# Performance work log

Hardware: AMD Instinct MI355X
Metric: run time of the kernel (lower is better)

The kernel has to match this reference:

```python
import jax, jax.numpy as jnp
import numpy as np

CH_IN = 256
CH_OUT = 32


def setup_inputs() -> dict:
    key = jax.random.key(0)
    ks = jax.random.split(key, 7)
    b, c, H, W = 4, CH_IN, 64, 64
    x = jax.random.normal(ks[0], (b, c, H, W), dtype=jnp.float32)
    # 1x1 conv weights (out, in) and biases, small init like torch default
    sc_in = 1.0 / np.sqrt(CH_IN)
    Wf = jax.random.uniform(ks[1], (CH_OUT, CH_IN), jnp.float32, -sc_in, sc_in)
    bf = jax.random.uniform(ks[2], (CH_OUT,), jnp.float32, -sc_in, sc_in)
    Wg = jax.random.uniform(ks[3], (CH_OUT, CH_IN), jnp.float32, -sc_in, sc_in)
    bg = jax.random.uniform(ks[4], (CH_OUT,), jnp.float32, -sc_in, sc_in)
    Wh = jax.random.uniform(ks[5], (CH_IN, CH_IN), jnp.float32, -sc_in, sc_in)
    bh = jax.random.uniform(ks[6], (CH_IN,), jnp.float32, -sc_in, sc_in)
    return {"x": x, "Wf": Wf, "bf": bf, "Wg": Wg, "bg": bg, "Wh": Wh, "bh": bh}


def reference(x, Wf, bf, Wg, bg, Wh, bh):
    b, c, H, W = x.shape
    xf = x.reshape(b, c, H * W)                      # [b, c, N]
    # 1x1 convs == per-pixel linear projections
    f = jnp.einsum('oc,bcn->bon', Wf, xf) + bf[None, :, None]   # [b, ch_out, N]
    g = jnp.einsum('oc,bcn->bon', Wg, xf) + bg[None, :, None]   # [b, ch_out, N]
    h = jnp.einsum('oc,bcn->bon', Wh, xf) + bh[None, :, None]   # [b, ch_in, N]
    # s[b, i, j] = sum_o f[b,o,i] * g[b,o,j]
    s = jnp.einsum('boi,boj->bij', f, g)             # [b, N, N]
    # torch softmax over dim=1 (the i axis)
    beta = jax.nn.softmax(s, axis=1)                 # [b, N, N]
    # o = h @ beta : [b, c, N] x [b, N, N] -> [b, c, N]
    o = jnp.einsum('bcn,bnm->bcm', h, beta)
    return o.reshape(b, c, H, W)
```

## Files before the change

### kernel.cpp

```cpp
#include <hip/hip_runtime.h>
#include <hip/hip_bf16.h>
#include <math.h>

#define BATCH 4
#define CIN   256
#define DQK   32
#define NPIX  4096
#define MTOT  320

typedef __attribute__((ext_vector_type(4))) float f32x4;
typedef __attribute__((ext_vector_type(8))) short bf16x8;
typedef __attribute__((ext_vector_type(4))) unsigned int u32x4;

__device__ __forceinline__ unsigned short f2bf(float f) {
  unsigned u = __builtin_bit_cast(unsigned, f);
  u += 0x7FFFu + ((u >> 16) & 1u);
  return (unsigned short)(u >> 16);
}
__device__ __forceinline__ unsigned pk2(float a, float b) {
  return (unsigned)f2bf(a) | ((unsigned)f2bf(b) << 16);
}
__device__ __forceinline__ void barrier_lds() {
  asm volatile("s_waitcnt lgkmcnt(0)" ::: "memory");
  __builtin_amdgcn_s_barrier();
  asm volatile("" ::: "memory");
}

__global__ void wcvt(const float* __restrict__ Wh, const float* __restrict__ Wf,
                     const float* __restrict__ Wg,
                     const float* __restrict__ bh, const float* __restrict__ bf,
                     const float* __restrict__ bg,
                     unsigned short* __restrict__ Wb, float* __restrict__ bcat) {
  const int r = blockIdx.x;
  const int c = threadIdx.x;
  const float* src = (r < 256) ? &Wh[r * CIN] : (r < 288) ? &Wf[(r - 256) * CIN] : &Wg[(r - 288) * CIN];
  Wb[r * CIN + c] = f2bf(src[c]);
  if (c == 0)
    bcat[r] = (r < 256) ? bh[r] : (r < 288) ? bf[r - 256] : bg[r - 288];
}

#define XPAD 4
__launch_bounds__(512, 1)
__global__ void proj_all(const float* __restrict__ x, const unsigned short* __restrict__ Wb,
                         const float* __restrict__ bcat,
                         unsigned short* __restrict__ F, unsigned short* __restrict__ G,
                         unsigned short* __restrict__ H) {
  __shared__ unsigned short Xs[64 * (CIN + XPAD)];

  const int bid = blockIdx.x;
  const int b = bid >> 6;
  const int n0 = (bid & 63) << 6;
  const int t = threadIdx.x;
  const int lane = t & 63;
  const int w = t >> 6;

  const float* __restrict__ xb = x + (size_t)b * CIN * NPIX + n0;
#pragma unroll
  for (int p = 0; p < 16; ++p) {
    const int k = p * 16 + w * 2;
    const float a0 = xb[(size_t)k * NPIX + lane];
    const float a1 = xb[(size_t)(k + 1) * NPIX + lane];
    const unsigned pk = (unsigned)f2bf(a0) | ((unsigned)f2bf(a1) << 16);
    *(unsigned*)((char*)Xs + lane * (CIN + XPAD) * 2 + k * 2) = pk;
  }
  __syncthreads();

  const int l16 = lane & 15, lhi = lane >> 4;
  const int wm = w >> 1;
  const int wn = w & 1;

  const f32x4 fzero = {0.f, 0.f, 0.f, 0.f};
  f32x4 acc[5][2];
#pragma unroll
  for (int i = 0; i < 5; ++i)
#pragma unroll
    for (int j = 0; j < 2; ++j) acc[i][j] = fzero;

#pragma unroll
  for (int ks = 0; ks < 8; ++ks) {
    bf16x8 bx[2];
#pragma unroll
    for (int j = 0; j < 2; ++j)
      bx[j] = *(const bf16x8*)&Xs[(wn * 32 + j * 16 + l16) * (CIN + XPAD) + ks * 32 + lhi * 8];
#pragma unroll
    for (int i = 0; i < 5; ++i) {
      const bf16x8 aw = *(const bf16x8*)(Wb + (size_t)(wm * 80 + i * 16 + l16) * CIN + ks * 32 + lhi * 8);
#pragma unroll
      for (int j = 0; j < 2; ++j)
        acc[i][j] = __builtin_amdgcn_mfma_f32_16x16x32_bf16(aw, bx[j], acc[i][j], 0, 0, 0);
    }
  }

#pragma unroll
  for (int i = 0; i < 5; ++i) {
    const int MT = wm * 5 + i;
    const int m0 = MT * 16;
    const f32x4 bias = *(const f32x4*)&bcat[m0 + lhi * 4];
#pragma unroll
    for (int j = 0; j < 2; ++j) {
      const int n = n0 + wn * 32 + j * 16 + l16;
      f32x4 v = acc[i][j];
      v.x += bias.x; v.y += bias.y; v.z += bias.z; v.w += bias.w;
      if (MT < 16) {
        const int c0 = m0 + lhi * 4;
        unsigned short* dst = H + ((size_t)b * CIN + c0) * NPIX + n;
        dst[0 * NPIX] = f2bf(v.x);
        dst[1 * NPIX] = f2bf(v.y);
        dst[2 * NPIX] = f2bf(v.z);
        dst[3 * NPIX] = f2bf(v.w);
      } else {
        unsigned short* dst = (MT < 18) ? F : G;
        const int d0 = ((MT - 16) & 1) * 16 + lhi * 4;
        uint2 pk;
        pk.x = (unsigned)f2bf(v.x) | ((unsigned)f2bf(v.y) << 16);
        pk.y = (unsigned)f2bf(v.z) | ((unsigned)f2bf(v.w) << 16);
        *(uint2*)(dst + ((size_t)b * NPIX + n) * DQK + d0) = pk;
      }
    }
  }
}

#define BNK  64
#define KEYS 2048
#define NTILE (KEYS / BNK)

__launch_bounds__(256, 2)
__global__ void attn_split(const unsigned short* __restrict__ F,
                           const unsigned short* __restrict__ G,
                           const unsigned short* __restrict__ H,
                           unsigned short* __restrict__ Ap, float* __restrict__ Lp) {
  __shared__ unsigned short Kl[2][64][36];
  __shared__ unsigned short Pl[2][64][72];

  const int bid = blockIdx.x;
  const int b = (bid & 7) >> 1;
  const int split = bid & 1;
  const int qt = bid >> 3;
  const int t = threadIdx.x;
  const int lane = t & 63, cs = t >> 6;
  const int l16 = lane & 15, lhi = lane >> 4;

  const unsigned short* Fb = F + (size_t)b * NPIX * DQK;
  const unsigned short* Gb = G + (size_t)b * NPIX * DQK;
  const unsigned short* Hb = H + (size_t)b * CIN * NPIX;
  const int nb0 = split * KEYS;
  const int q0 = qt * 64;

  const f32x4 fzero = {0.f, 0.f, 0.f, 0.f};

  bf16x8 qf[4];
#pragma unroll
  for (int mt = 0; mt < 4; ++mt)
    qf[mt] = *(const bf16x8*)(Gb + (size_t)(q0 + mt * 16 + l16) * DQK + lhi * 8);

  f32x4 acc[4][4];
#pragma unroll
  for (int ct = 0; ct < 4; ++ct)
#pragma unroll
    for (int mt = 0; mt < 4; ++mt) acc[ct][mt] = fzero;
  float Lacc[4] = {0.f, 0.f, 0.f, 0.f};

  const int krow = t >> 2, kslot = t & 3;
  const unsigned short* Kg = Fb + ((size_t)(nb0 + krow)) * DQK + kslot * 8;
  const unsigned short* vp[4];
#pragma unroll
  for (int ct = 0; ct < 4; ++ct)
    vp[ct] = Hb + (size_t)(cs * 64 + ct * 16 + l16) * NPIX + nb0 + lhi * 8;

  u32x4 kr;
  kr = *(const u32x4*)Kg;
  *(u32x4*)&Kl[0][krow][kslot * 8] = kr;
  kr = *(const u32x4*)(Kg + 1 * BNK * DQK);
  barrier_lds();

  for (int tt = 0; tt < NTILE; ++tt) {
    const int buf = tt & 1;
    u32x4 vr[8];
#pragma unroll
    for (int ct = 0; ct < 4; ++ct)
#pragma unroll
      for (int kk = 0; kk < 2; ++kk)
        vr[ct * 2 + kk] = *(const u32x4*)(vp[ct] + (size_t)tt * BNK + kk * 32);
    if (tt + 1 < NTILE) *(u32x4*)&Kl[buf ^ 1][krow][kslot * 8] = kr;
    if (tt + 2 < NTILE) kr = *(const u32x4*)(Kg + (size_t)(tt + 2) * BNK * DQK);

    const bf16x8 kf = *(const bf16x8*)&Kl[buf][cs * 16 + l16][lhi * 8];
    f32x4 s_[4];
#pragma unroll
    for (int mt = 0; mt < 4; ++mt)
      s_[mt] = __builtin_amdgcn_mfma_f32_16x16x32_bf16(kf, qf[mt], fzero, 0, 0, 0);

#pragma unroll
    for (int mt = 0; mt < 4; ++mt) {
      const float p0 = __expf(s_[mt][0]), p1 = __expf(s_[mt][1]);
      const float p2 = __expf(s_[mt][2]), p3 = __expf(s_[mt][3]);
      Lacc[mt] += (p0 + p1) + (p2 + p3);
      uint2 pk; pk.x = pk2(p0, p1); pk.y = pk2(p2, p3);
      *(uint2*)&Pl[buf][mt * 16 + l16][cs * 16 + lhi * 4] = pk;
    }
    barrier_lds();

    __builtin_amdgcn_s_setprio(1);
#pragma unroll
    for (int kk = 0; kk < 2; ++kk) {
      bf16x8 pf[4];
#pragma unroll
      for (int mt = 0; mt < 4; ++mt)
        pf[mt] = *(const bf16x8*)&Pl[buf][mt * 16 + l16][kk * 32 + lhi * 8];
#pragma unroll
      for (int ct = 0; ct < 4; ++ct) {
        const bf16x8 vf = __builtin_bit_cast(bf16x8, vr[ct * 2 + kk]);
#pragma unroll
        for (int mt = 0; mt < 4; ++mt)
          acc[ct][mt] = __builtin_amdgcn_mfma_f32_16x16x32_bf16(vf, pf[mt], acc[ct][mt], 0, 0, 0);
      }
    }
    __builtin_amdgcn_s_setprio(0);
  }

#pragma unroll
  for (int mt = 0; mt < 4; ++mt) {
    float L = Lacc[mt];
    L += __shfl_xor(L, 16, 64);
    L += __shfl_xor(L, 32, 64);
    if (lhi == 0)
      Lp[((size_t)split * 4 + cs) * (4 * NPIX) + (size_t)b * NPIX + q0 + mt * 16 + l16] = L;
  }
#pragma unroll
  for (int ct = 0; ct < 4; ++ct)
#pragma unroll
    for (int mt = 0; mt < 4; ++mt) {
      const int c = cs * 64 + ct * 16 + lhi * 4;
      const int q = q0 + mt * 16 + l16;
      unsigned short* dst = Ap + (((size_t)split * 4 + b) * CIN + c) * NPIX + q;
#pragma unroll
      for (int v = 0; v < 4; ++v) dst[(size_t)v * NPIX] = f2bf(acc[ct][mt][v]);
    }
}

__global__ void combineL(const float* __restrict__ Lp, float* __restrict__ Linv) {
  const int idx = blockIdx.x * 256 + threadIdx.x;
  float s = 0.f;
#pragma unroll
  for (int i = 0; i < 8; ++i) s += Lp[(size_t)i * (4 * NPIX) + idx];
  Linv[idx] = 1.f / s;
}

__global__ void combine(const unsigned short* __restrict__ Ap, const float* __restrict__ Linv,
                        float* __restrict__ out) {
  const size_t base = ((size_t)blockIdx.x * 256 + threadIdx.x) * 8;
  const int b = (int)(base / ((size_t)CIN * NPIX));
  const int q = (int)(base % NPIX);
  const u32x4 a0 = *(const u32x4*)(Ap + base);
  const u32x4 a1 = *(const u32x4*)(Ap + (size_t)4 * CIN * NPIX + base);
  const float* lv = &Linv[(size_t)b * NPIX + q];
  float r[8];
#pragma unroll
  for (int i = 0; i < 4; ++i) {
    const float x0 = __builtin_bit_cast(float, (a0[i] & 0xFFFFu) << 16) +
                     __builtin_bit_cast(float, (a1[i] & 0xFFFFu) << 16);
    const float x1 = __builtin_bit_cast(float, (a0[i] & 0xFFFF0000u)) +
                     __builtin_bit_cast(float, (a1[i] & 0xFFFF0000u));
    r[2 * i] = x0 * lv[2 * i];
    r[2 * i + 1] = x1 * lv[2 * i + 1];
  }
  *(f32x4*)&out[base] = *(f32x4*)&r[0];
  *(f32x4*)&out[base + 4] = *(f32x4*)&r[4];
}

#define BN 32
__launch_bounds__(512, 2)
__global__ void attn_kernel(const unsigned short* __restrict__ F,
                            const unsigned short* __restrict__ G,
                            const unsigned short* __restrict__ H,
                            float* __restrict__ out) {
  __shared__ unsigned short Klds[32 * 40];
  __shared__ unsigned short Vlds[256 * 40];
  __shared__ unsigned short Plds[8][32 * 40];

  const int bid = blockIdx.x;
  const int b = bid >> 6;
  const int t = threadIdx.x;
  const int lane = t & 63;
  const int w = t >> 6;
  const int l16 = lane & 15;
  const int lhi = lane >> 4;
  const int m0 = ((bid & 63) << 6) + ((w >> 2) << 5);
  const int c0 = (w & 3) << 6;

  const f32x4 fzero = {0.f, 0.f, 0.f, 0.f};

  bf16x8 qf[2];
#pragma unroll
  for (int mt = 0; mt < 2; ++mt)
    qf[mt] = *(const bf16x8*)(G + ((size_t)b * NPIX + m0 + mt * 16 + l16) * DQK + lhi * 8);

  f32x4 acc[4][2];
#pragma unroll
  for (int ct = 0; ct < 4; ++ct)
#pragma unroll
    for (int mt = 0; mt < 2; ++mt) acc[ct][mt] = fzero;
  float Mr[2] = {-INFINITY, -INFINITY};
  float Lr[2] = {0.f, 0.f};

  const unsigned short* Fb = F + (size_t)b * NPIX * DQK;
  const unsigned short* Hb = H + (size_t)b * CIN * NPIX;
  unsigned short* Pw = &Plds[w][0];

  for (int n0 = 0; n0 < NPIX; n0 += BN) {
    __syncthreads();
    if (t < 128) {
      const int nr = t >> 2, sl = t & 3;
      *(u32x4*)&Klds[nr * 40 + sl * 8] = *(const u32x4*)(Fb + (size_t)(n0 + nr) * DQK + sl * 8);
    }
#pragma unroll
    for (int i = 0; i < 2; ++i) {
      const int q = t + i * 512;
      const int cr = q >> 2, sl = q & 3;
      *(u32x4*)&Vlds[cr * 40 + sl * 8] = *(const u32x4*)(Hb + (size_t)cr * NPIX + n0 + sl * 8);
    }
    __syncthreads();

    bf16x8 kf[2];
#pragma unroll
    for (int nts = 0; nts < 2; ++nts)
      kf[nts] = *(const bf16x8*)&Klds[(nts * 16 + l16) * 40 + lhi * 8];
    f32x4 s[2][2];
#pragma unroll
    for (int mt = 0; mt < 2; ++mt)
#pragma unroll
      for (int nts = 0; nts < 2; ++nts)
        s[mt][nts] = __builtin_amdgcn_mfma_f32_16x16x32_bf16(kf[nts], qf[mt], fzero, 0, 0, 0);

#pragma unroll
    for (int mt = 0; mt < 2; ++mt) {
      float tmax = s[mt][0][0];
#pragma unroll
      for (int v = 1; v < 4; ++v) tmax = fmaxf(tmax, s[mt][0][v]);
#pragma unroll
      for (int v = 0; v < 4; ++v) tmax = fmaxf(tmax, s[mt][1][v]);
      tmax = fmaxf(tmax, __shfl_xor(tmax, 16, 64));
      tmax = fmaxf(tmax, __shfl_xor(tmax, 32, 64));
      const float newM = fmaxf(Mr[mt], tmax);
      const float rescale = __expf(Mr[mt] - newM);
      Mr[mt] = newM;
      float p[2][4];
      float psum = 0.f;
#pragma unroll
      for (int nts = 0; nts < 2; ++nts)
#pragma unroll
        for (int v = 0; v < 4; ++v) {
          p[nts][v] = __expf(s[mt][nts][v] - newM);
          psum += p[nts][v];
        }
      psum += __shfl_xor(psum, 16, 64);
      psum += __shfl_xor(psum, 32, 64);
      Lr[mt] = Lr[mt] * rescale + psum;
#pragma unroll
      for (int ct = 0; ct < 4; ++ct) acc[ct][mt] *= rescale;
#pragma unroll
      for (int nts = 0; nts < 2; ++nts) {
        uint2 pkv;
        pkv.x = (unsigned)f2bf(p[nts][0]) | ((unsigned)f2bf(p[nts][1]) << 16);
        pkv.y = (unsigned)f2bf(p[nts][2]) | ((unsigned)f2bf(p[nts][3]) << 16);
        *(uint2*)&Pw[(mt * 16 + l16) * 40 + nts * 16 + lhi * 4] = pkv;
      }
    }
    asm volatile("" ::: "memory");

    bf16x8 pf[2];
#pragma unroll
    for (int mt = 0; mt < 2; ++mt)
      pf[mt] = *(const bf16x8*)&Pw[(mt * 16 + l16) * 40 + lhi * 8];
#pragma unroll
    for (int ct = 0; ct < 4; ++ct) {
      const bf16x8 vf = *(const bf16x8*)&Vlds[(c0 + ct * 16 + l16) * 40 + lhi * 8];
#pragma unroll
      for (int mt = 0; mt < 2; ++mt)
        acc[ct][mt] = __builtin_amdgcn_mfma_f32_16x16x32_bf16(vf, pf[mt], acc[ct][mt], 0, 0, 0);
    }
  }

#pragma unroll
  for (int mt = 0; mt < 2; ++mt) {
    const float invL = 1.f / Lr[mt];
    const int m = m0 + mt * 16 + l16;
#pragma unroll
    for (int ct = 0; ct < 4; ++ct)
#pragma unroll
      for (int v = 0; v < 4; ++v) {
        const int c = c0 + ct * 16 + lhi * 4 + v;
        out[((size_t)b * CIN + c) * NPIX + m] = acc[ct][mt][v] * invL;
      }
  }
}

extern "C" void kernel_launch(void* const* d_in, const int* in_sizes, int n_in,
                              void* d_out, int out_size, void* d_ws, size_t ws_size,
                              hipStream_t stream) {
  (void)in_sizes; (void)n_in; (void)out_size;
  const float* x  = (const float*)d_in[0];
  const float* Wf = (const float*)d_in[1];
  const float* bf = (const float*)d_in[2];
  const float* Wg = (const float*)d_in[3];
  const float* bg = (const float*)d_in[4];
  const float* Wh = (const float*)d_in[5];
  const float* bh = (const float*)d_in[6];
  float* out = (float*)d_out;

  unsigned short* Fw = (unsigned short*)d_ws;
  unsigned short* Gw = Fw + (size_t)BATCH * NPIX * DQK;
  unsigned short* Hw = Gw + (size_t)BATCH * NPIX * DQK;
  unsigned short* Wb = Hw + (size_t)BATCH * CIN * NPIX;
  float* bcat = (float*)(Wb + (size_t)MTOT * CIN);
  unsigned short* Apart = (unsigned short*)(bcat + MTOT);
  float* Lpart = (float*)(Apart + (size_t)2 * BATCH * CIN * NPIX);
  float* Linv  = Lpart + (size_t)8 * BATCH * NPIX;
  const size_t NEED = (size_t)((char*)(Linv + (size_t)BATCH * NPIX) - (char*)d_ws);

  hipLaunchKernelGGL(wcvt, dim3(MTOT), dim3(256), 0, stream, Wh, Wf, Wg, bh, bf, bg, Wb, bcat);
  hipLaunchKernelGGL(proj_all, dim3(BATCH * 64), dim3(512), 0, stream, x, Wb, bcat, Fw, Gw, Hw);

  if (ws_size >= NEED) {
    hipLaunchKernelGGL(attn_split, dim3(BATCH * 64 * 2), dim3(256), 0, stream, Fw, Gw, Hw, Apart, Lpart);
    hipLaunchKernelGGL(combineL, dim3(BATCH * NPIX / 256), dim3(256), 0, stream, Lpart, Linv);
    hipLaunchKernelGGL(combine, dim3((size_t)BATCH * CIN * NPIX / 8 / 256), dim3(256), 0, stream, Apart, Linv, out);
  } else {
    hipLaunchKernelGGL(attn_kernel, dim3(BATCH * 64), dim3(512), 0, stream, Fw, Gw, Hw, out);
  }
}
```

Baseline: 99.10 us.

## Stage V tiles in shared LDS across two query-group waves per block

```diff
diff --git a/kernel.cpp b/kernel.cpp
--- a/kernel.cpp
+++ b/kernel.cpp
@@ -124,102 +124,104 @@
 #define KEYS 2048
 #define NTILE (KEYS / BNK)
 
-__launch_bounds__(256, 2)
+__launch_bounds__(512, 4)
 __global__ void attn_split(const unsigned short* __restrict__ F,
                            const unsigned short* __restrict__ G,
                            const unsigned short* __restrict__ H,
                            unsigned short* __restrict__ Ap, float* __restrict__ Lp) {
-  __shared__ unsigned short Kl[2][64][36];
-  __shared__ unsigned short Pl[2][64][72];
+  __shared__ unsigned short Kl[64][36];
+  __shared__ unsigned short Vl[256][72];
+  __shared__ unsigned short Pl[2][32][72];
 
   const int bid = blockIdx.x;
-  const int b = (bid & 7) >> 1;
+  const int b = (bid >> 1) & 3;
   const int split = bid & 1;
   const int qt = bid >> 3;
   const int t = threadIdx.x;
-  const int lane = t & 63, cs = t >> 6;
+  const int lane = t & 63, w = t >> 6;
   const int l16 = lane & 15, lhi = lane >> 4;
+  const int mg = w >> 2, cs = w & 3;
 
   const unsigned short* Fb = F + (size_t)b * NPIX * DQK;
   const unsigned short* Gb = G + (size_t)b * NPIX * DQK;
   const unsigned short* Hb = H + (size_t)b * CIN * NPIX;
   const int nb0 = split * KEYS;
-  const int q0 = qt * 64;
+  const int q0 = qt * 64 + mg * 32;
 
   const f32x4 fzero = {0.f, 0.f, 0.f, 0.f};
 
-  bf16x8 qf[4];
-#pragma unroll
-  for (int mt = 0; mt < 4; ++mt)
+  bf16x8 qf[2];
+#pragma unroll
+  for (int mt = 0; mt < 2; ++mt)
     qf[mt] = *(const bf16x8*)(Gb + (size_t)(q0 + mt * 16 + l16) * DQK + lhi * 8);
 
-  f32x4 acc[4][4];
+  f32x4 acc[4][2];
 #pragma unroll
   for (int ct = 0; ct < 4; ++ct)
 #pragma unroll
-    for (int mt = 0; mt < 4; ++mt) acc[ct][mt] = fzero;
-  float Lacc[4] = {0.f, 0.f, 0.f, 0.f};
-
+    for (int mt = 0; mt < 2; ++mt) acc[ct][mt] = fzero;
+  float Lacc[2] = {0.f, 0.f};
+
+  const int vrow = t >> 3, vslot = t & 7;
   const int krow = t >> 2, kslot = t & 3;
-  const unsigned short* Kg = Fb + ((size_t)(nb0 + krow)) * DQK + kslot * 8;
-  const unsigned short* vp[4];
-#pragma unroll
-  for (int ct = 0; ct < 4; ++ct)
-    vp[ct] = Hb + (size_t)(cs * 64 + ct * 16 + l16) * NPIX + nb0 + lhi * 8;
-
-  u32x4 kr;
-  kr = *(const u32x4*)Kg;
-  *(u32x4*)&Kl[0][krow][kslot * 8] = kr;
-  kr = *(const u32x4*)(Kg + 1 * BNK * DQK);
-  barrier_lds();
+  const unsigned short* Vg = Hb + (size_t)vrow * NPIX + nb0 + vslot * 8;
+  const unsigned short* Kg = Fb + (size_t)(nb0 + krow) * DQK + kslot * 8;
+
+  u32x4 vr[4];
+  u32x4 kr = {0, 0, 0, 0};
+
+#pragma unroll
+  for (int i = 0; i < 4; ++i)
+    vr[i] = *(const u32x4*)(Vg + (size_t)i * 64 * NPIX);
+  if (t < 256) kr = *(const u32x4*)Kg;
 
   for (int tt = 0; tt < NTILE; ++tt) {
-    const int buf = tt & 1;
-    u32x4 vr[8];
-#pragma unroll
-    for (int ct = 0; ct < 4; ++ct)
-#pragma unroll
-      for (int kk = 0; kk < 2; ++kk)
-        vr[ct * 2 + kk] = *(const u32x4*)(vp[ct] + (size_t)tt * BNK + kk * 32);
-    if (tt + 1 < NTILE) *(u32x4*)&Kl[buf ^ 1][krow][kslot * 8] = kr;
-    if (tt + 2 < NTILE) kr = *(const u32x4*)(Kg + (size_t)(tt + 2) * BNK * DQK);
-
-    const bf16x8 kf = *(const bf16x8*)&Kl[buf][cs * 16 + l16][lhi * 8];
-    f32x4 s_[4];
-#pragma unroll
-    for (int mt = 0; mt < 4; ++mt)
+#pragma unroll
+    for (int i = 0; i < 4; ++i)
+      *(u32x4*)&Vl[i * 64 + vrow][vslot * 8] = vr[i];
+    if (t < 256) *(u32x4*)&Kl[krow][kslot * 8] = kr;
+    barrier_lds();
+    if (tt + 1 < NTILE) {
+#pragma unroll
+      for (int i = 0; i < 4; ++i)
+        vr[i] = *(const u32x4*)(Vg + (size_t)i * 64 * NPIX + (size_t)(tt + 1) * BNK);
+      if (t < 256) kr = *(const u32x4*)(Kg + (size_t)(tt + 1) * BNK * DQK);
+    }
+    const bf16x8 kf = *(const bf16x8*)&Kl[cs * 16 + l16][lhi * 8];
+    f32x4 s_[2];
+#pragma unroll
+    for (int mt = 0; mt < 2; ++mt)
       s_[mt] = __builtin_amdgcn_mfma_f32_16x16x32_bf16(kf, qf[mt], fzero, 0, 0, 0);
-
-#pragma unroll
-    for (int mt = 0; mt < 4; ++mt) {
+#pragma unroll
+    for (int mt = 0; mt < 2; ++mt) {
       const float p0 = __expf(s_[mt][0]), p1 = __expf(s_[mt][1]);
       const float p2 = __expf(s_[mt][2]), p3 = __expf(s_[mt][3]);
       Lacc[mt] += (p0 + p1) + (p2 + p3);
       uint2 pk; pk.x = pk2(p0, p1); pk.y = pk2(p2, p3);
-      *(uint2*)&Pl[buf][mt * 16 + l16][cs * 16 + lhi * 4] = pk;
+      *(uint2*)&Pl[mg][mt * 16 + l16][cs * 16 + lhi * 4] = pk;
     }
     barrier_lds();
-
     __builtin_amdgcn_s_setprio(1);
 #pragma unroll
     for (int kk = 0; kk < 2; ++kk) {
-      bf16x8 pf[4];
-#pragma unroll
-      for (int mt = 0; mt < 4; ++mt)
-        pf[mt] = *(const bf16x8*)&Pl[buf][mt * 16 + l16][kk * 32 + lhi * 8];
+      bf16x8 pf[2];
+#pragma unroll
+      for (int mt = 0; mt < 2; ++mt)
+        pf[mt] = *(const bf16x8*)&Pl[mg][mt * 16 + l16][kk * 32 + lhi * 8];
 #pragma unroll
       for (int ct = 0; ct < 4; ++ct) {
-        const bf16x8 vf = __builtin_bit_cast(bf16x8, vr[ct * 2 + kk]);
-#pragma unroll
-        for (int mt = 0; mt < 4; ++mt)
+        const bf16x8 vf = *(const bf16x8*)&Vl[cs * 64 + ct * 16 + l16][kk * 32 + lhi * 8];
+#pragma unroll
+        for (int mt = 0; mt < 2; ++mt)
           acc[ct][mt] = __builtin_amdgcn_mfma_f32_16x16x32_bf16(vf, pf[mt], acc[ct][mt], 0, 0, 0);
       }
     }
     __builtin_amdgcn_s_setprio(0);
-  }
-
-#pragma unroll
-  for (int mt = 0; mt < 4; ++mt) {
+    barrier_lds();
+  }
+
+#pragma unroll
+  for (int mt = 0; mt < 2; ++mt) {
     float L = Lacc[mt];
     L += __shfl_xor(L, 16, 64);
     L += __shfl_xor(L, 32, 64);
@@ -229,7 +231,7 @@
 #pragma unroll
   for (int ct = 0; ct < 4; ++ct)
 #pragma unroll
-    for (int mt = 0; mt < 4; ++mt) {
+    for (int mt = 0; mt < 2; ++mt) {
       const int c = cs * 64 + ct * 16 + lhi * 4;
       const int q = q0 + mt * 16 + l16;
       unsigned short* dst = Ap + (((size_t)split * 4 + b) * CIN + c) * NPIX + q;
@@ -422,7 +424,7 @@
   hipLaunchKernelGGL(proj_all, dim3(BATCH * 64), dim3(512), 0, stream, x, Wb, bcat, Fw, Gw, Hw);
 
   if (ws_size >= NEED) {
-    hipLaunchKernelGGL(attn_split, dim3(BATCH * 64 * 2), dim3(256), 0, stream, Fw, Gw, Hw, Apart, Lpart);
+    hipLaunchKernelGGL(attn_split, dim3(BATCH * 64 * 2), dim3(512), 0, stream, Fw, Gw, Hw, Apart, Lpart);
     hipLaunchKernelGGL(combineL, dim3(BATCH * NPIX / 256), dim3(256), 0, stream, Lpart, Linv);
     hipLaunchKernelGGL(combine, dim3((size_t)BATCH * CIN * NPIX / 8 / 256), dim3(256), 0, stream, Apart, Linv, out);
   } else {
```

Measured after the change: 95.29 us. 1.04x faster.

## Load K fragments directly to registers and double-buffer V/K register prefetch

Applied to the files above, without the earlier changes.

```diff
diff --git a/kernel.cpp b/kernel.cpp
--- a/kernel.cpp
+++ b/kernel.cpp
@@ -129,11 +129,10 @@
                            const unsigned short* __restrict__ G,
                            const unsigned short* __restrict__ H,
                            unsigned short* __restrict__ Ap, float* __restrict__ Lp) {
-  __shared__ unsigned short Kl[2][64][36];
-  __shared__ unsigned short Pl[2][64][72];
+  __shared__ unsigned short Pl[64][72];
 
   const int bid = blockIdx.x;
-  const int b = (bid & 7) >> 1;
+  const int b = (bid >> 1) & 3;
   const int split = bid & 1;
   const int qt = bid >> 3;
   const int t = threadIdx.x;
@@ -160,63 +159,66 @@
     for (int mt = 0; mt < 4; ++mt) acc[ct][mt] = fzero;
   float Lacc[4] = {0.f, 0.f, 0.f, 0.f};
 
-  const int krow = t >> 2, kslot = t & 3;
-  const unsigned short* Kg = Fb + ((size_t)(nb0 + krow)) * DQK + kslot * 8;
-  const unsigned short* vp[4];
+  const unsigned short* Kp = Fb + (size_t)(nb0 + cs * 16 + l16) * DQK + lhi * 8;
+  const unsigned short* Vp[4];
 #pragma unroll
   for (int ct = 0; ct < 4; ++ct)
-    vp[ct] = Hb + (size_t)(cs * 64 + ct * 16 + l16) * NPIX + nb0 + lhi * 8;
-
-  u32x4 kr;
-  kr = *(const u32x4*)Kg;
-  *(u32x4*)&Kl[0][krow][kslot * 8] = kr;
-  kr = *(const u32x4*)(Kg + 1 * BNK * DQK);
-  barrier_lds();
-
-  for (int tt = 0; tt < NTILE; ++tt) {
-    const int buf = tt & 1;
-    u32x4 vr[8];
-#pragma unroll
-    for (int ct = 0; ct < 4; ++ct)
-#pragma unroll
-      for (int kk = 0; kk < 2; ++kk)
-        vr[ct * 2 + kk] = *(const u32x4*)(vp[ct] + (size_t)tt * BNK + kk * 32);
-    if (tt + 1 < NTILE) *(u32x4*)&Kl[buf ^ 1][krow][kslot * 8] = kr;
-    if (tt + 2 < NTILE) kr = *(const u32x4*)(Kg + (size_t)(tt + 2) * BNK * DQK);
-
-    const bf16x8 kf = *(const bf16x8*)&Kl[buf][cs * 16 + l16][lhi * 8];
-    f32x4 s_[4];
-#pragma unroll
-    for (int mt = 0; mt < 4; ++mt)
-      s_[mt] = __builtin_amdgcn_mfma_f32_16x16x32_bf16(kf, qf[mt], fzero, 0, 0, 0);
-
-#pragma unroll
-    for (int mt = 0; mt < 4; ++mt) {
-      const float p0 = __expf(s_[mt][0]), p1 = __expf(s_[mt][1]);
-      const float p2 = __expf(s_[mt][2]), p3 = __expf(s_[mt][3]);
-      Lacc[mt] += (p0 + p1) + (p2 + p3);
-      uint2 pk; pk.x = pk2(p0, p1); pk.y = pk2(p2, p3);
-      *(uint2*)&Pl[buf][mt * 16 + l16][cs * 16 + lhi * 4] = pk;
-    }
-    barrier_lds();
-
-    __builtin_amdgcn_s_setprio(1);
-#pragma unroll
-    for (int kk = 0; kk < 2; ++kk) {
-      bf16x8 pf[4];
-#pragma unroll
-      for (int mt = 0; mt < 4; ++mt)
-        pf[mt] = *(const bf16x8*)&Pl[buf][mt * 16 + l16][kk * 32 + lhi * 8];
-#pragma unroll
-      for (int ct = 0; ct < 4; ++ct) {
-        const bf16x8 vf = __builtin_bit_cast(bf16x8, vr[ct * 2 + kk]);
-#pragma unroll
-        for (int mt = 0; mt < 4; ++mt)
-          acc[ct][mt] = __builtin_amdgcn_mfma_f32_16x16x32_bf16(vf, pf[mt], acc[ct][mt], 0, 0, 0);
-      }
-    }
-    __builtin_amdgcn_s_setprio(0);
-  }
+    Vp[ct] = Hb + (size_t)(cs * 64 + ct * 16 + l16) * NPIX + nb0 + lhi * 8;
+
+  u32x4 vA[8], vB[8], kA, kB;
+
+#define LOADT(VR, KR, TT) do {                                                       \
+    _Pragma("unroll")                                                                \
+    for (int ct_ = 0; ct_ < 4; ++ct_)                                                \
+      _Pragma("unroll")                                                              \
+      for (int kk_ = 0; kk_ < 2; ++kk_)                                              \
+        VR[ct_ * 2 + kk_] = *(const u32x4*)(Vp[ct_] + (size_t)(TT) * BNK + kk_ * 32);\
+    KR = *(const u32x4*)(Kp + (size_t)(TT) * BNK * DQK);                             \
+  } while (0)
+
+#define COMPUTE(VR, KR) do {                                                         \
+    const bf16x8 kf_ = __builtin_bit_cast(bf16x8, KR);                               \
+    f32x4 s_[4];                                                                     \
+    _Pragma("unroll")                                                                \
+    for (int mt_ = 0; mt_ < 4; ++mt_)                                                \
+      s_[mt_] = __builtin_amdgcn_mfma_f32_16x16x32_bf16(kf_, qf[mt_], fzero, 0, 0, 0);\
+    _Pragma("unroll")                                                                \
+    for (int mt_ = 0; mt_ < 4; ++mt_) {                                              \
+      const float p0 = __expf(s_[mt_][0]), p1 = __expf(s_[mt_][1]);                  \
+      const float p2 = __expf(s_[mt_][2]), p3 = __expf(s_[mt_][3]);                  \
+      Lacc[mt_] += (p0 + p1) + (p2 + p3);                                            \
+      uint2 pk_; pk_.x = pk2(p0, p1); pk_.y = pk2(p2, p3);                           \
+      *(uint2*)&Pl[mt_ * 16 + l16][cs * 16 + lhi * 4] = pk_;                         \
+    }                                                                                \
+    barrier_lds();                                                \
+    __builtin_amdgcn_s_setprio(1);                                                   \
+    _Pragma("unroll")                                                                \
+    for (int kk_ = 0; kk_ < 2; ++kk_) {                                              \
+      bf16x8 pf_[4];                                                                 \
+      _Pragma("unroll")                                                              \
+      for (int mt_ = 0; mt_ < 4; ++mt_)                                              \
+        pf_[mt_] = *(const bf16x8*)&Pl[mt_ * 16 + l16][kk_ * 32 + lhi * 8];          \
+      _Pragma("unroll")                                                              \
+      for (int ct_ = 0; ct_ < 4; ++ct_) {                                            \
+        const bf16x8 vf_ = __builtin_bit_cast(bf16x8, VR[ct_ * 2 + kk_]);            \
+        _Pragma("unroll")                                                            \
+        for (int mt_ = 0; mt_ < 4; ++mt_)                                            \
+          acc[ct_][mt_] = __builtin_amdgcn_mfma_f32_16x16x32_bf16(vf_, pf_[mt_], acc[ct_][mt_], 0, 0, 0); \
+      }                                                                              \
+    }                                                                                \
+    __builtin_amdgcn_s_setprio(0);                                                   \
+    barrier_lds();                          \
+  } while (0)
+
+  LOADT(vA, kA, 0);
+  for (int tt = 0; tt < NTILE; tt += 2) {
+    if (tt + 1 < NTILE) LOADT(vB, kB, tt + 1);
+    COMPUTE(vA, kA);
+    if (tt + 2 < NTILE) LOADT(vA, kA, tt + 2);
+    COMPUTE(vB, kB);
+  }
+#undef LOADT
+#undef COMPUTE
 
 #pragma unroll
   for (int mt = 0; mt < 4; ++mt) {
```

Result: slower. 107.7 us (+8.7%).

## Stage V tiles in LDS shared by two query groups and software-pipeline QK

Applied to the files above, without the earlier changes.

```diff
diff --git a/kernel.cpp b/kernel.cpp
--- a/kernel.cpp
+++ b/kernel.cpp
@@ -124,27 +124,30 @@
 #define KEYS 2048
 #define NTILE (KEYS / BNK)
 
-__launch_bounds__(256, 2)
+__launch_bounds__(512, 2)
 __global__ void attn_split(const unsigned short* __restrict__ F,
                            const unsigned short* __restrict__ G,
                            const unsigned short* __restrict__ H,
                            unsigned short* __restrict__ Ap, float* __restrict__ Lp) {
-  __shared__ unsigned short Kl[2][64][36];
-  __shared__ unsigned short Pl[2][64][72];
+  __shared__ unsigned short Kl[2][64][40];
+  __shared__ unsigned short Vl[2][256][72];
+  __shared__ unsigned short Pl[2][2][64][72];
 
   const int bid = blockIdx.x;
-  const int b = (bid & 7) >> 1;
-  const int split = bid & 1;
+  const int slab = bid & 7;
+  const int b = slab >> 1;
+  const int split = slab & 1;
   const int qt = bid >> 3;
   const int t = threadIdx.x;
-  const int lane = t & 63, cs = t >> 6;
+  const int lane = t & 63, w = t >> 6;
   const int l16 = lane & 15, lhi = lane >> 4;
+  const int mg = w >> 2, cs = w & 3;
 
   const unsigned short* Fb = F + (size_t)b * NPIX * DQK;
   const unsigned short* Gb = G + (size_t)b * NPIX * DQK;
   const unsigned short* Hb = H + (size_t)b * CIN * NPIX;
   const int nb0 = split * KEYS;
-  const int q0 = qt * 64;
+  const int q0 = qt * 128 + mg * 64;
 
   const f32x4 fzero = {0.f, 0.f, 0.f, 0.f};
 
@@ -160,63 +163,78 @@
     for (int mt = 0; mt < 4; ++mt) acc[ct][mt] = fzero;
   float Lacc[4] = {0.f, 0.f, 0.f, 0.f};
 
+  const int vrow = t >> 3, vslot = t & 7;
   const int krow = t >> 2, kslot = t & 3;
-  const unsigned short* Kg = Fb + ((size_t)(nb0 + krow)) * DQK + kslot * 8;
-  const unsigned short* vp[4];
-#pragma unroll
-  for (int ct = 0; ct < 4; ++ct)
-    vp[ct] = Hb + (size_t)(cs * 64 + ct * 16 + l16) * NPIX + nb0 + lhi * 8;
-
-  u32x4 kr;
-  kr = *(const u32x4*)Kg;
-  *(u32x4*)&Kl[0][krow][kslot * 8] = kr;
-  kr = *(const u32x4*)(Kg + 1 * BNK * DQK);
+  const unsigned short* Vg = Hb + (size_t)vrow * NPIX + nb0 + vslot * 8;
+  const unsigned short* Kg = Fb + (size_t)(nb0 + krow) * DQK + kslot * 8;
+
+  u32x4 vr[4];
+  u32x4 kr = {0, 0, 0, 0};
+
+#define LOADT(TT) do {                                                          \
+    _Pragma("unroll")                                                           \
+    for (int i_ = 0; i_ < 4; ++i_)                                              \
+      vr[i_] = *(const u32x4*)(Vg + (size_t)i_ * 64 * NPIX + (size_t)(TT) * BNK);\
+    if (t < 256) kr = *(const u32x4*)(Kg + (size_t)(TT) * BNK * DQK);           \
+  } while (0)
+
+#define STORET(BUF) do {                                                        \
+    _Pragma("unroll")                                                           \
+    for (int i_ = 0; i_ < 4; ++i_)                                              \
+      *(u32x4*)&Vl[BUF][i_ * 64 + vrow][vslot * 8] = vr[i_];                    \
+    if (t < 256) *(u32x4*)&Kl[BUF][krow][kslot * 8] = kr;                       \
+  } while (0)
+
+#define QKSM(BUF, PAR) do {                                                     \
+    const bf16x8 kf_ = *(const bf16x8*)&Kl[BUF][cs * 16 + l16][lhi * 8];        \
+    f32x4 s_[4];                                                                \
+    _Pragma("unroll")                                                           \
+    for (int mt_ = 0; mt_ < 4; ++mt_)                                           \
+      s_[mt_] = __builtin_amdgcn_mfma_f32_16x16x32_bf16(kf_, qf[mt_], fzero, 0, 0, 0); \
+    _Pragma("unroll")                                                           \
+    for (int mt_ = 0; mt_ < 4; ++mt_) {                                         \
+      const float p0 = __expf(s_[mt_][0]), p1 = __expf(s_[mt_][1]);             \
+      const float p2 = __expf(s_[mt_][2]), p3 = __expf(s_[mt_][3]);             \
+      Lacc[mt_] += (p0 + p1) + (p2 + p3);                                       \
+      uint2 pk_; pk_.x = pk2(p0, p1); pk_.y = pk2(p2, p3);                      \
+      *(uint2*)&Pl[PAR][mg][mt_ * 16 + l16][cs * 16 + lhi * 4] = pk_;           \
+    }                                                                           \
+  } while (0)
+
+  LOADT(0); STORET(0);
+  LOADT(1); STORET(1);
+  LOADT(2);
   barrier_lds();
+  QKSM(0, 0);
 
   for (int tt = 0; tt < NTILE; ++tt) {
     const int buf = tt & 1;
-    u32x4 vr[8];
-#pragma unroll
-    for (int ct = 0; ct < 4; ++ct)
+    barrier_lds();
+    bf16x8 pf[4][2];
+#pragma unroll
+    for (int mt = 0; mt < 4; ++mt)
 #pragma unroll
       for (int kk = 0; kk < 2; ++kk)
-        vr[ct * 2 + kk] = *(const u32x4*)(vp[ct] + (size_t)tt * BNK + kk * 32);
-    if (tt + 1 < NTILE) *(u32x4*)&Kl[buf ^ 1][krow][kslot * 8] = kr;
-    if (tt + 2 < NTILE) kr = *(const u32x4*)(Kg + (size_t)(tt + 2) * BNK * DQK);
-
-    const bf16x8 kf = *(const bf16x8*)&Kl[buf][cs * 16 + l16][lhi * 8];
-    f32x4 s_[4];
-#pragma unroll
-    for (int mt = 0; mt < 4; ++mt)
-      s_[mt] = __builtin_amdgcn_mfma_f32_16x16x32_bf16(kf, qf[mt], fzero, 0, 0, 0);
-
-#pragma unroll
-    for (int mt = 0; mt < 4; ++mt) {
-      const float p0 = __expf(s_[mt][0]), p1 = __expf(s_[mt][1]);
-      const float p2 = __expf(s_[mt][2]), p3 = __expf(s_[mt][3]);
-      Lacc[mt] += (p0 + p1) + (p2 + p3);
-      uint2 pk; pk.x = pk2(p0, p1); pk.y = pk2(p2, p3);
-      *(uint2*)&Pl[buf][mt * 16 + l16][cs * 16 + lhi * 4] = pk;
-    }
+        pf[mt][kk] = *(const bf16x8*)&Pl[buf][mg][mt * 16 + l16][kk * 32 + lhi * 8];
+    if (tt + 1 < NTILE) QKSM(buf ^ 1, buf ^ 1);
+    __builtin_amdgcn_s_setprio(1);
+#pragma unroll
+    for (int kk = 0; kk < 2; ++kk)
+#pragma unroll
+      for (int ct = 0; ct < 4; ++ct) {
+        const bf16x8 vf = *(const bf16x8*)&Vl[buf][cs * 64 + ct * 16 + l16][kk * 32 + lhi * 8];
+#pragma unroll
+        for (int mt = 0; mt < 4; ++mt)
+          acc[ct][mt] = __builtin_amdgcn_mfma_f32_16x16x32_bf16(vf, pf[mt][kk], acc[ct][mt], 0, 0, 0);
+      }
+    __builtin_amdgcn_s_setprio(0);
     barrier_lds();
-
-    __builtin_amdgcn_s_setprio(1);
-#pragma unroll
-    for (int kk = 0; kk < 2; ++kk) {
-      bf16x8 pf[4];
-#pragma unroll
-      for (int mt = 0; mt < 4; ++mt)
-        pf[mt] = *(const bf16x8*)&Pl[buf][mt * 16 + l16][kk * 32 + lhi * 8];
-#pragma unroll
-      for (int ct = 0; ct < 4; ++ct) {
-        const bf16x8 vf = __builtin_bit_cast(bf16x8, vr[ct * 2 + kk]);
-#pragma unroll
-        for (int mt = 0; mt < 4; ++mt)
-          acc[ct][mt] = __builtin_amdgcn_mfma_f32_16x16x32_bf16(vf, pf[mt], acc[ct][mt], 0, 0, 0);
-      }
-    }
-    __builtin_amdgcn_s_setprio(0);
-  }
+    if (tt + 2 < NTILE) STORET(buf);
+    if (tt + 3 < NTILE) LOADT(tt + 3);
+  }
+#undef LOADT
+#undef STORET
+#undef QKSM
 
 #pragma unroll
   for (int mt = 0; mt < 4; ++mt) {
@@ -422,7 +440,7 @@
   hipLaunchKernelGGL(proj_all, dim3(BATCH * 64), dim3(512), 0, stream, x, Wb, bcat, Fw, Gw, Hw);
 
   if (ws_size >= NEED) {
-    hipLaunchKernelGGL(attn_split, dim3(BATCH * 64 * 2), dim3(256), 0, stream, Fw, Gw, Hw, Apart, Lpart);
+    hipLaunchKernelGGL(attn_split, dim3(BATCH * 32 * 2), dim3(512), 0, stream, Fw, Gw, Hw, Apart, Lpart);
     hipLaunchKernelGGL(combineL, dim3(BATCH * NPIX / 256), dim3(256), 0, stream, Lpart, Linv);
     hipLaunchKernelGGL(combine, dim3((size_t)BATCH * CIN * NPIX / 8 / 256), dim3(256), 0, stream, Apart, Linv, out);
   } else {
```

Measured after the change: 87.50 us. 11.7% less time.
